# Performance work log

Hardware: AMD Instinct MI355X
Metric: run time of the kernel (lower is better)

The kernel has to match this reference:

```python
import jax, jax.numpy as jnp
import numpy as np

EPS = 1e-5  # BatchNorm eps

def _gcn_norm(edge_index, edge_weight, n):
    # PyG gcn_norm with add_self_loops=True, fill_value=1.0
    loop = jnp.arange(n, dtype=edge_index.dtype)
    row = jnp.concatenate([edge_index[0], loop])
    col = jnp.concatenate([edge_index[1], loop])
    ew = jnp.concatenate([edge_weight, jnp.ones((n,), edge_weight.dtype)])
    deg = jax.ops.segment_sum(ew, col, num_segments=n)
    dis = jnp.where(deg > 0, jax.lax.rsqrt(jnp.maximum(deg, 1e-30)), 0.0)
    norm = dis[row] * ew * dis[col]
    return row, col, norm

def _gcn_conv(x, W, b, row, col, norm, n):
    h = x @ W                               # [N, out]
    msg = h[row] * norm[:, None]            # gather + edge scale
    out = jax.ops.segment_sum(msg, col, num_segments=n)
    return out + b

def _bn_eval(x, gamma, beta, mean, var):
    return (x - mean) * jax.lax.rsqrt(var + EPS) * gamma + beta

def setup_inputs() -> dict:
    key = jax.random.key(0)
    ks = jax.random.split(key, 12)
    N, E, V, H = 100000, 1600000, 256, 128
    x = jax.random.normal(ks[0], (N, V), jnp.float32)
    edge_index = jax.random.randint(ks[1], (2, E), 0, N, jnp.int64)
    edge_weight = jax.random.uniform(ks[2], (E,), jnp.float32)
    s = lambda fan: 1.0 / np.sqrt(fan)
    return {
        "x": x, "edge_index": edge_index, "edge_weight": edge_weight,
        "W1": jax.random.normal(ks[3], (V, H), jnp.float32) * s(V),
        "b1": jnp.zeros((H,), jnp.float32),
        "W2": jax.random.normal(ks[4], (H, H), jnp.float32) * s(H),
        "b2": jnp.zeros((H,), jnp.float32),
        "W3": jax.random.normal(ks[5], (H, 1), jnp.float32) * s(H),
        "b3": jnp.zeros((1,), jnp.float32),
        "Wres": jax.random.normal(ks[6], (V, H), jnp.float32) * s(V),
        "g1": jnp.ones((H,), jnp.float32), "be1": jnp.zeros((H,), jnp.float32),
        "m1": jax.random.normal(ks[7], (H,), jnp.float32) * 0.01,
        "v1": jnp.ones((H,), jnp.float32),
        "g2": jnp.ones((H,), jnp.float32), "be2": jnp.zeros((H,), jnp.float32),
        "m2": jax.random.normal(ks[8], (H,), jnp.float32) * 0.01,
        "v2": jnp.ones((H,), jnp.float32),
    }

def reference(x, edge_index, edge_weight, W1, b1, W2, b2, W3, b3, Wres,
              g1, be1, m1, v1, g2, be2, m2, v2):
    n = x.shape[0]
    row, col, norm = _gcn_norm(edge_index, edge_weight, n)
    res = x @ Wres                                   # residual branch
    h = _gcn_conv(x, W1, b1, row, col, norm, n)
    h = jax.nn.relu(_bn_eval(h, g1, be1, m1, v1))    # dropout off (eval)
    h = _gcn_conv(h, W2, b2, row, col, norm, n) + res
    h = jax.nn.relu(_bn_eval(h, g2, be2, m2, v2))
    h = _gcn_conv(h, W3, b3, row, col, norm, n)      # [N, 1]
    return jnp.squeeze(h, axis=1)
```

## Files before the change

### kernel.cpp

```cpp
#include <hip/hip_runtime.h>
#include <hip/hip_bf16.h>

#define BN_EPS 1e-5f

using short8 = __attribute__((ext_vector_type(8))) short;
using f32x4  = __attribute__((ext_vector_type(4))) float;

#define FIX_SCALE 1048576.0f
#define FIX_MASK  ((1ULL << 42) - 1)
#define CNT_ONE   (1ULL << 42)

static __device__ __forceinline__ unsigned short f2bf(float f) {
  unsigned int u = __float_as_uint(f);
  unsigned int r = (u + 0x7fffu + ((u >> 16) & 1u)) >> 16;
  return (unsigned short)r;
}


static __global__ void hist_kernel(const int* __restrict__ col,
                                   const float* __restrict__ ew,
                                   unsigned long long* __restrict__ packed, int E) {
  int e = blockIdx.x * blockDim.x + threadIdx.x;
  if (e < E) {
    int c = col[e];
    unsigned long long fx = (unsigned long long)(unsigned int)(ew[e] * FIX_SCALE + 0.5f);
    atomicAdd(&packed[c], CNT_ONE | fx);
  }
}

static __global__ void unpack_kernel(const unsigned long long* __restrict__ packed,
                                     float* __restrict__ dis, int* __restrict__ cnt, int N) {
  int i = blockIdx.x * blockDim.x + threadIdx.x;
  if (i < N) {
    unsigned long long v = packed[i];
    cnt[i] = (int)(v >> 42);
    float deg = 1.0f + (float)(v & FIX_MASK) * (1.0f / FIX_SCALE);
    dis[i] = rsqrtf(deg);
  }
}

#define SCAN_B 256
#define SCAN_I 4
static __global__ void scanA(const int* __restrict__ cnt, int* __restrict__ start,
                             int* __restrict__ blkSum, int N) {
  __shared__ int sh[SCAN_B];
  int t = threadIdx.x;
  int base = blockIdx.x * SCAN_B * SCAN_I + t * SCAN_I;
  int v[SCAN_I];
  int tot = 0;
#pragma unroll
  for (int j = 0; j < SCAN_I; ++j) {
    v[j] = (base + j < N) ? cnt[base + j] : 0;
    tot += v[j];
  }
  sh[t] = tot;
  __syncthreads();
  int self = tot;
  for (int off = 1; off < SCAN_B; off <<= 1) {
    int add = (t >= off) ? sh[t - off] : 0;
    __syncthreads();
    sh[t] += add;
    __syncthreads();
  }
  int excl = sh[t] - self;
  if (t == SCAN_B - 1) blkSum[blockIdx.x] = sh[t];
  int run = excl;
#pragma unroll
  for (int j = 0; j < SCAN_I; ++j) {
    if (base + j < N) start[base + j] = run;
    run += v[j];
  }
}

static __global__ void scanB(const int* __restrict__ blkSum, int* __restrict__ blkOff, int nb) {
  __shared__ int sh[256];
  int t = threadIdx.x;
  int v = (t < nb) ? blkSum[t] : 0;
  sh[t] = v;
  __syncthreads();
  for (int off = 1; off < 256; off <<= 1) {
    int add = (t >= off) ? sh[t - off] : 0;
    __syncthreads();
    sh[t] += add;
    __syncthreads();
  }
  if (t < nb) blkOff[t] = sh[t] - v;
}

static __global__ void scanC(int* start, int* cursor, const int* __restrict__ blkOff, int N) {
  int i = blockIdx.x * blockDim.x + threadIdx.x;
  if (i < N) {
    int s = start[i] + blkOff[i / (SCAN_B * SCAN_I)];
    start[i] = s;
    cursor[i] = s;
  }
}

static __global__ void scatter_kernel(const int* __restrict__ row, const int* __restrict__ col,
                                      const float* __restrict__ ew, const float* __restrict__ dis,
                                      int* cursor, int2* __restrict__ edges, int E) {
  int e = blockIdx.x * blockDim.x + threadIdx.x;
  if (e < E) {
    int r = row[e], c = col[e];
    int pos = atomicAdd(&cursor[c], 1);
    float nrm = dis[r] * ew[e] * dis[c];
    edges[pos] = make_int2(r, __float_as_int(nrm));
  }
}


static __global__ void cast_weights(const float* __restrict__ W1, const float* __restrict__ Wres,
                                    const float* __restrict__ W2,
                                    unsigned short* __restrict__ BT1,
                                    unsigned short* __restrict__ BT2) {
  int i = blockIdx.x * blockDim.x + threadIdx.x;
  if (i < 256 * 256) {
    int n = i >> 8, k = i & 255;
    float v = (n < 128) ? W1[k * 128 + n] : Wres[k * 128 + (n - 128)];
    BT1[i] = f2bf(v);
  } else if (i < 256 * 256 + 128 * 128) {
    int j = i - 256 * 256;
    int n = j >> 7, k = j & 127;
    BT2[j] = f2bf(W2[k * 128 + n]);
  }
}


static __global__ __launch_bounds__(256)
void gemm1_mfma(const float* __restrict__ A, const unsigned short* __restrict__ BT,
                unsigned short* __restrict__ C0, float* __restrict__ C1, int M) {
  __shared__ unsigned short As[64 * 40];
  __shared__ unsigned short Bs[256 * 40];
  int t = threadIdx.x;
  int wv = t >> 6, lane = t & 63;
  int quad = lane >> 4, l15 = lane & 15;
  int m0 = blockIdx.x * 64;

  f32x4 acc[4][4];
#pragma unroll
  for (int i = 0; i < 4; ++i)
#pragma unroll
    for (int j = 0; j < 4; ++j) acc[i][j] = (f32x4){0.f, 0.f, 0.f, 0.f};

  int ar = t >> 2;
  int ac = (t & 3) * 8;
  bool avalid = (m0 + ar) < M;
  const float* Arow = A + (size_t)(m0 + ar) * 256 + ac;
  const unsigned short* Brow = BT + (size_t)t * 256;

  for (int k0 = 0; k0 < 256; k0 += 32) {
    float4 a0 = make_float4(0.f, 0.f, 0.f, 0.f), a1 = a0;
    if (avalid) {
      a0 = *(const float4*)(Arow + k0);
      a1 = *(const float4*)(Arow + k0 + 4);
    }
    short8 av;
    av[0] = (short)f2bf(a0.x); av[1] = (short)f2bf(a0.y);
    av[2] = (short)f2bf(a0.z); av[3] = (short)f2bf(a0.w);
    av[4] = (short)f2bf(a1.x); av[5] = (short)f2bf(a1.y);
    av[6] = (short)f2bf(a1.z); av[7] = (short)f2bf(a1.w);
    *(short8*)&As[ar * 40 + ac] = av;

    short8 b0 = *(const short8*)(Brow + k0);
    short8 b1 = *(const short8*)(Brow + k0 + 8);
    short8 b2 = *(const short8*)(Brow + k0 + 16);
    short8 b3 = *(const short8*)(Brow + k0 + 24);
    *(short8*)&Bs[t * 40 + 0]  = b0;
    *(short8*)&Bs[t * 40 + 8]  = b1;
    *(short8*)&Bs[t * 40 + 16] = b2;
    *(short8*)&Bs[t * 40 + 24] = b3;
    __syncthreads();

    short8 af[4], bf[4];
#pragma unroll
    for (int mt = 0; mt < 4; ++mt)
      af[mt] = *(const short8*)&As[(mt * 16 + l15) * 40 + quad * 8];
#pragma unroll
    for (int nt = 0; nt < 4; ++nt)
      bf[nt] = *(const short8*)&Bs[(wv * 64 + nt * 16 + l15) * 40 + quad * 8];
#pragma unroll
    for (int mt = 0; mt < 4; ++mt)
#pragma unroll
      for (int nt = 0; nt < 4; ++nt)
        acc[mt][nt] = __builtin_amdgcn_mfma_f32_16x16x32_bf16(af[mt], bf[nt], acc[mt][nt], 0, 0, 0);
    __syncthreads();
  }

  int nbase = wv * 64;
#pragma unroll
  for (int mt = 0; mt < 4; ++mt) {
#pragma unroll
    for (int nt = 0; nt < 4; ++nt) {
      int n = nbase + nt * 16 + l15;
#pragma unroll
      for (int reg = 0; reg < 4; ++reg) {
        size_t m = (size_t)(m0 + mt * 16 + quad * 4 + reg);
        if (nbase < 128) C0[m * 128 + n] = f2bf(acc[mt][nt][reg]);
        else             C1[m * 128 + (n - 128)] = acc[mt][nt][reg];
      }
    }
  }
}


static __global__ __launch_bounds__(256)
void gemm2_mfma(const unsigned short* __restrict__ A, const unsigned short* __restrict__ BT,
                unsigned short* __restrict__ C, int Mp) {
  __shared__ unsigned short As[128 * 40];
  __shared__ unsigned short Bs[128 * 40];
  int t = threadIdx.x;
  int wv = t >> 6, lane = t & 63;
  int quad = lane >> 4, l15 = lane & 15;
  int m0 = blockIdx.x * 128;

  f32x4 acc[4][4];
#pragma unroll
  for (int i = 0; i < 4; ++i)
#pragma unroll
    for (int j = 0; j < 4; ++j) acc[i][j] = (f32x4){0.f, 0.f, 0.f, 0.f};

  int sr = t >> 1, sc = (t & 1) * 16;

  for (int k0 = 0; k0 < 128; k0 += 32) {
    short8 a0 = *(const short8*)(A + (size_t)(m0 + sr) * 128 + k0 + sc);
    short8 a1 = *(const short8*)(A + (size_t)(m0 + sr) * 128 + k0 + sc + 8);
    *(short8*)&As[sr * 40 + sc]     = a0;
    *(short8*)&As[sr * 40 + sc + 8] = a1;
    short8 b0 = *(const short8*)(BT + (size_t)sr * 128 + k0 + sc);
    short8 b1 = *(const short8*)(BT + (size_t)sr * 128 + k0 + sc + 8);
    *(short8*)&Bs[sr * 40 + sc]     = b0;
    *(short8*)&Bs[sr * 40 + sc + 8] = b1;
    __syncthreads();

    int mb = (wv >> 1) * 64, nb = (wv & 1) * 64;
    short8 af[4], bf[4];
#pragma unroll
    for (int mt = 0; mt < 4; ++mt)
      af[mt] = *(const short8*)&As[(mb + mt * 16 + l15) * 40 + quad * 8];
#pragma unroll
    for (int nt = 0; nt < 4; ++nt)
      bf[nt] = *(const short8*)&Bs[(nb + nt * 16 + l15) * 40 + quad * 8];
#pragma unroll
    for (int mt = 0; mt < 4; ++mt)
#pragma unroll
      for (int nt = 0; nt < 4; ++nt)
        acc[mt][nt] = __builtin_amdgcn_mfma_f32_16x16x32_bf16(af[mt], bf[nt], acc[mt][nt], 0, 0, 0);
    __syncthreads();
  }

  int mb = (wv >> 1) * 64, nb = (wv & 1) * 64;
#pragma unroll
  for (int mt = 0; mt < 4; ++mt)
#pragma unroll
    for (int nt = 0; nt < 4; ++nt) {
      int n = nb + nt * 16 + l15;
#pragma unroll
      for (int reg = 0; reg < 4; ++reg) {
        size_t m = (size_t)(m0 + mb + mt * 16 + quad * 4 + reg);
        C[m * 128 + n] = f2bf(acc[mt][nt][reg]);
      }
    }
  (void)Mp;
}


#define PROP_GATHER_BODY                                                        \
  int c0 = lane * 2;                                                            \
  float d = dis[w];                                                             \
  float d2 = d * d;                                                             \
  float acc0, acc1;                                                             \
  {                                                                             \
    unsigned int u = Hsrc[(size_t)w * 64 + lane];                               \
    acc0 = d2 * __uint_as_float(u << 16);                                       \
    acc1 = d2 * __uint_as_float(u & 0xffff0000u);                               \
  }                                                                             \
  int s = start[w], n = cnt[w];                                                 \
  int k = 0;                                                                    \
  while (k < n) {                                                               \
    int chunk = min(n - k, 64);                                                 \
    int idx = 0;                                                                \
    float wt = 0.f;                                                             \
    if (lane < chunk) {                                                         \
      int2 ev = edges[s + k + lane];                                            \
      idx = ev.x;                                                               \
      wt  = __int_as_float(ev.y);                                               \
    }                                                                           \
    for (int j = 0; j < chunk; j += 8) {                                        \
      int   i0 = __shfl(idx, j + 0, 64), i1 = __shfl(idx, j + 1, 64);           \
      int   i2 = __shfl(idx, j + 2, 64), i3 = __shfl(idx, j + 3, 64);           \
      int   i4 = __shfl(idx, j + 4, 64), i5 = __shfl(idx, j + 5, 64);           \
      int   i6 = __shfl(idx, j + 6, 64), i7 = __shfl(idx, j + 7, 64);           \
      float w0 = __shfl(wt, j + 0, 64), w1 = __shfl(wt, j + 1, 64);             \
      float w2 = __shfl(wt, j + 2, 64), w3 = __shfl(wt, j + 3, 64);             \
      float w4 = __shfl(wt, j + 4, 64), w5 = __shfl(wt, j + 5, 64);             \
      float w6 = __shfl(wt, j + 6, 64), w7 = __shfl(wt, j + 7, 64);             \
      unsigned int u0 = Hsrc[(size_t)i0 * 64 + lane];                           \
      unsigned int u1 = Hsrc[(size_t)i1 * 64 + lane];                           \
      unsigned int u2 = Hsrc[(size_t)i2 * 64 + lane];                           \
      unsigned int u3 = Hsrc[(size_t)i3 * 64 + lane];                           \
      unsigned int u4 = Hsrc[(size_t)i4 * 64 + lane];                           \
      unsigned int u5 = Hsrc[(size_t)i5 * 64 + lane];                           \
      unsigned int u6 = Hsrc[(size_t)i6 * 64 + lane];                           \
      unsigned int u7 = Hsrc[(size_t)i7 * 64 + lane];                           \
      acc0 = fmaf(w0, __uint_as_float(u0 << 16), acc0);                         \
      acc1 = fmaf(w0, __uint_as_float(u0 & 0xffff0000u), acc1);                 \
      acc0 = fmaf(w1, __uint_as_float(u1 << 16), acc0);                         \
      acc1 = fmaf(w1, __uint_as_float(u1 & 0xffff0000u), acc1);                 \
      acc0 = fmaf(w2, __uint_as_float(u2 << 16), acc0);                         \
      acc1 = fmaf(w2, __uint_as_float(u2 & 0xffff0000u), acc1);                 \
      acc0 = fmaf(w3, __uint_as_float(u3 << 16), acc0);                         \
      acc1 = fmaf(w3, __uint_as_float(u3 & 0xffff0000u), acc1);                 \
      acc0 = fmaf(w4, __uint_as_float(u4 << 16), acc0);                         \
      acc1 = fmaf(w4, __uint_as_float(u4 & 0xffff0000u), acc1);                 \
      acc0 = fmaf(w5, __uint_as_float(u5 << 16), acc0);                         \
      acc1 = fmaf(w5, __uint_as_float(u5 & 0xffff0000u), acc1);                 \
      acc0 = fmaf(w6, __uint_as_float(u6 << 16), acc0);                         \
      acc1 = fmaf(w6, __uint_as_float(u6 & 0xffff0000u), acc1);                 \
      acc0 = fmaf(w7, __uint_as_float(u7 << 16), acc0);                         \
      acc1 = fmaf(w7, __uint_as_float(u7 & 0xffff0000u), acc1);                 \
    }                                                                           \
    k += chunk;                                                                 \
  }

static __global__ __launch_bounds__(256)
void prop128_bf16out(const unsigned int* __restrict__ Hsrc,
                     const int* __restrict__ start, const int* __restrict__ cnt,
                     const int2* __restrict__ edges,
                     const float* __restrict__ dis,
                     const float* __restrict__ bvec,
                     const float* __restrict__ g, const float* __restrict__ be,
                     const float* __restrict__ mean, const float* __restrict__ var,
                     unsigned int* __restrict__ Outb, int N) {
  int w = (int)((blockIdx.x * blockDim.x + threadIdx.x) >> 6);
  int lane = threadIdx.x & 63;
  if (w >= N) return;
  PROP_GATHER_BODY
  float x0 = acc0 + bvec[c0];
  float x1 = acc1 + bvec[c0 + 1];
  float s0 = g[c0] * rsqrtf(var[c0] + BN_EPS);
  float s1 = g[c0 + 1] * rsqrtf(var[c0 + 1] + BN_EPS);
  x0 = fmaxf((x0 - mean[c0]) * s0 + be[c0], 0.f);
  x1 = fmaxf((x1 - mean[c0 + 1]) * s1 + be[c0 + 1], 0.f);
  unsigned int packed = (unsigned int)f2bf(x0) | ((unsigned int)f2bf(x1) << 16);
  Outb[(size_t)w * 64 + lane] = packed;
}

static __global__ __launch_bounds__(256)
void prop128_w3out(const unsigned int* __restrict__ Hsrc,
                   const int* __restrict__ start, const int* __restrict__ cnt,
                   const int2* __restrict__ edges,
                   const float* __restrict__ dis,
                   const float* __restrict__ bvec,
                   const float* __restrict__ g, const float* __restrict__ be,
                   const float* __restrict__ mean, const float* __restrict__ var,
                   const float* __restrict__ res, const float* __restrict__ W3,
                   float* __restrict__ h3, int N) {
  int w = (int)((blockIdx.x * blockDim.x + threadIdx.x) >> 6);
  int lane = threadIdx.x & 63;
  if (w >= N) return;
  PROP_GATHER_BODY
  float x0 = acc0 + bvec[c0] + res[(size_t)w * 128 + c0];
  float x1 = acc1 + bvec[c0 + 1] + res[(size_t)w * 128 + c0 + 1];
  float s0 = g[c0] * rsqrtf(var[c0] + BN_EPS);
  float s1 = g[c0 + 1] * rsqrtf(var[c0 + 1] + BN_EPS);
  x0 = fmaxf((x0 - mean[c0]) * s0 + be[c0], 0.f);
  x1 = fmaxf((x1 - mean[c0 + 1]) * s1 + be[c0 + 1], 0.f);
  float v = x0 * W3[c0] + x1 * W3[c0 + 1];
#pragma unroll
  for (int off = 32; off > 0; off >>= 1) v += __shfl_down(v, off, 64);
  if (lane == 0) h3[w] = v;
}


static __global__ void prop3_kernel(const float* __restrict__ h3,
                                    const int* __restrict__ start, const int* __restrict__ cnt,
                                    const int2* __restrict__ edges,
                                    const float* __restrict__ dis, const float* __restrict__ b3,
                                    float* __restrict__ out, int N) {
  int i = blockIdx.x * blockDim.x + threadIdx.x;
  if (i >= N) return;
  float d = dis[i];
  float acc = d * d * h3[i];
  int s = start[i], n = cnt[i];
  for (int k = 0; k < n; ++k) {
    int2 ev = edges[s + k];
    acc = fmaf(__int_as_float(ev.y), h3[ev.x], acc);
  }
  out[i] = acc + b3[0];
}


extern "C" void kernel_launch(void* const* d_in, const int* in_sizes, int n_in,
                              void* d_out, int out_size, void* d_ws, size_t ws_size,
                              hipStream_t stream) {
  const float* x    = (const float*)d_in[0];
  const int*   ei   = (const int*)d_in[1];
  const float* ew   = (const float*)d_in[2];
  const float* W1   = (const float*)d_in[3];
  const float* b1   = (const float*)d_in[4];
  const float* W2   = (const float*)d_in[5];
  const float* b2   = (const float*)d_in[6];
  const float* W3   = (const float*)d_in[7];
  const float* b3   = (const float*)d_in[8];
  const float* Wres = (const float*)d_in[9];
  const float* g1   = (const float*)d_in[10];
  const float* be1  = (const float*)d_in[11];
  const float* m1   = (const float*)d_in[12];
  const float* v1   = (const float*)d_in[13];
  const float* g2   = (const float*)d_in[14];
  const float* be2  = (const float*)d_in[15];
  const float* m2   = (const float*)d_in[16];
  const float* v2   = (const float*)d_in[17];

  int Hh = in_sizes[4];
  int V  = in_sizes[3] / Hh;
  int N  = in_sizes[0] / V;
  int E  = in_sizes[2];
  const int* row = ei;
  const int* col = ei + E;

  int Mp = ((N + 127) / 128) * 128;

  char* p = (char*)d_ws;
  auto alloc = [&](size_t bytes) -> char* {
    char* r = p;
    p += (bytes + 255) & ~(size_t)255;
    return r;
  };
  unsigned long long* packed = (unsigned long long*)alloc((size_t)N * 8);
  float* dis    = (float*)alloc((size_t)N * 4);
  int*   cnt    = (int*)  alloc((size_t)N * 4);
  int*   startA = (int*)  alloc((size_t)N * 4);
  int*   cursor = (int*)  alloc((size_t)N * 4);
  int*   blkSum = (int*)  alloc(256 * 4);
  int*   blkOff = (int*)  alloc(256 * 4);
  int2*  edges  = (int2*) alloc((size_t)E * 8);
  float* h3     = (float*)alloc((size_t)N * 4);
  unsigned short* BT1 = (unsigned short*)alloc((size_t)256 * 256 * 2);
  unsigned short* BT2 = (unsigned short*)alloc((size_t)128 * 128 * 2);
  unsigned short* bufG  = (unsigned short*)alloc((size_t)Mp * 128 * 2);
  unsigned short* bufH1 = (unsigned short*)alloc((size_t)Mp * 128 * 2);
  float* bufRes = (float*)alloc((size_t)Mp * 128 * 4);
  (void)ws_size; (void)n_in; (void)out_size;

  int TB = 256;
  hipMemsetAsync(packed, 0, (size_t)N * 8, stream);
  hist_kernel<<<(E + TB - 1) / TB, TB, 0, stream>>>(col, ew, packed, E);
  unpack_kernel<<<(N + TB - 1) / TB, TB, 0, stream>>>(packed, dis, cnt, N);

  int nb = (N + SCAN_B * SCAN_I - 1) / (SCAN_B * SCAN_I);
  scanA<<<nb, SCAN_B, 0, stream>>>(cnt, startA, blkSum, N);
  scanB<<<1, 256, 0, stream>>>(blkSum, blkOff, nb);
  scanC<<<(N + TB - 1) / TB, TB, 0, stream>>>(startA, cursor, blkOff, N);
  scatter_kernel<<<(E + TB - 1) / TB, TB, 0, stream>>>(row, col, ew, dis, cursor, edges, E);

  cast_weights<<<(256 * 256 + 128 * 128 + TB - 1) / TB, TB, 0, stream>>>(W1, Wres, W2, BT1, BT2);

  gemm1_mfma<<<Mp / 64, 256, 0, stream>>>(x, BT1, bufG, bufRes, N);

  int propBlocks = (int)(((size_t)N * 64 + TB - 1) / TB);
  prop128_bf16out<<<propBlocks, TB, 0, stream>>>((const unsigned int*)bufG, startA, cnt,
                                                 edges, dis, b1, g1, be1, m1, v1,
                                                 (unsigned int*)bufH1, N);

  gemm2_mfma<<<Mp / 128, 256, 0, stream>>>(bufH1, BT2, bufG, Mp);

  prop128_w3out<<<propBlocks, TB, 0, stream>>>((const unsigned int*)bufG, startA, cnt,
                                               edges, dis, b2, g2, be2, m2, v2,
                                               bufRes, W3, h3, N);

  prop3_kernel<<<(N + TB - 1) / TB, TB, 0, stream>>>(h3, startA, cnt, edges,
                                                     dis, b3, (float*)d_out, N);
}
```

Measured before the change: 553.4 us.

## Capture per-edge rank in histogram atomics and drop scatter atomics in CSR build

The histogram atomic now returns the previous count, and that value is stored as a 16-bit rank for each edge. The placement kernel then computes each edge's slot as start plus rank instead of doing a second atomicAdd on a cursor array, and writes it with a nontemporal store. The destination-side dis factor is moved out of the per-edge weight and applied once per node after aggregation. Together these remove E contended atomics and a cursor array, at the cost of an extra E*2-byte rank buffer; rank is truncated to 16 bits, which is only safe for in-degrees below 65536.

```diff
diff --git a/kernel.cpp b/kernel.cpp
--- a/kernel.cpp
+++ b/kernel.cpp
@@ -19,12 +19,14 @@
 
 static __global__ void hist_kernel(const int* __restrict__ col,
                                    const float* __restrict__ ew,
-                                   unsigned long long* __restrict__ packed, int E) {
+                                   unsigned long long* __restrict__ packed,
+                                   unsigned short* __restrict__ rank, int E) {
   int e = blockIdx.x * blockDim.x + threadIdx.x;
   if (e < E) {
     int c = col[e];
     unsigned long long fx = (unsigned long long)(unsigned int)(ew[e] * FIX_SCALE + 0.5f);
-    atomicAdd(&packed[c], CNT_ONE | fx);
+    unsigned long long old = atomicAdd(&packed[c], CNT_ONE | fx);
+    rank[e] = (unsigned short)(old >> 42);
   }
 }
 
@@ -87,24 +89,23 @@
   if (t < nb) blkOff[t] = sh[t] - v;
 }
 
-static __global__ void scanC(int* start, int* cursor, const int* __restrict__ blkOff, int N) {
+static __global__ void scanC(int* start, const int* __restrict__ blkOff, int N) {
   int i = blockIdx.x * blockDim.x + threadIdx.x;
-  if (i < N) {
-    int s = start[i] + blkOff[i / (SCAN_B * SCAN_I)];
-    start[i] = s;
-    cursor[i] = s;
-  }
-}
-
-static __global__ void scatter_kernel(const int* __restrict__ row, const int* __restrict__ col,
-                                      const float* __restrict__ ew, const float* __restrict__ dis,
-                                      int* cursor, int2* __restrict__ edges, int E) {
+  if (i < N) start[i] += blkOff[i / (SCAN_B * SCAN_I)];
+}
+
+static __global__ void place_kernel(const int* __restrict__ row, const int* __restrict__ col,
+                                    const float* __restrict__ ew, const float* __restrict__ dis,
+                                    const int* __restrict__ start,
+                                    const unsigned short* __restrict__ rank,
+                                    long long* __restrict__ edges, int E) {
   int e = blockIdx.x * blockDim.x + threadIdx.x;
   if (e < E) {
     int r = row[e], c = col[e];
-    int pos = atomicAdd(&cursor[c], 1);
-    float nrm = dis[r] * ew[e] * dis[c];
-    edges[pos] = make_int2(r, __float_as_int(nrm));
+    int pos = start[c] + (int)rank[e];
+    float nrm = dis[r] * ew[e];
+    long long v = ((long long)__float_as_int(nrm) << 32) | (unsigned int)r;
+    __builtin_nontemporal_store(v, &edges[pos]);
   }
 }
 
@@ -267,12 +268,11 @@
 #define PROP_GATHER_BODY                                                        \
   int c0 = lane * 2;                                                            \
   float d = dis[w];                                                             \
-  float d2 = d * d;                                                             \
   float acc0, acc1;                                                             \
   {                                                                             \
     unsigned int u = Hsrc[(size_t)w * 64 + lane];                               \
-    acc0 = d2 * __uint_as_float(u << 16);                                       \
-    acc1 = d2 * __uint_as_float(u & 0xffff0000u);                               \
+    acc0 = d * __uint_as_float(u << 16);                                        \
+    acc1 = d * __uint_as_float(u & 0xffff0000u);                                \
   }                                                                             \
   int s = start[w], n = cnt[w];                                                 \
   int k = 0;                                                                    \
@@ -281,9 +281,9 @@
     int idx = 0;                                                                \
     float wt = 0.f;                                                             \
     if (lane < chunk) {                                                         \
-      int2 ev = edges[s + k + lane];                                            \
-      idx = ev.x;                                                               \
-      wt  = __int_as_float(ev.y);                                               \
+      long long ev = edges[s + k + lane];                                       \
+      idx = (int)(unsigned int)(ev & 0xffffffffLL);                             \
+      wt  = __int_as_float((int)(ev >> 32));                                    \
     }                                                                           \
     for (int j = 0; j < chunk; j += 8) {                                        \
       int   i0 = __shfl(idx, j + 0, 64), i1 = __shfl(idx, j + 1, 64);           \
@@ -320,12 +320,14 @@
       acc1 = fmaf(w7, __uint_as_float(u7 & 0xffff0000u), acc1);                 \
     }                                                                           \
     k += chunk;                                                                 \
-  }
+  }                                                                             \
+  acc0 *= d;                                                                    \
+  acc1 *= d;
 
 static __global__ __launch_bounds__(256)
 void prop128_bf16out(const unsigned int* __restrict__ Hsrc,
                      const int* __restrict__ start, const int* __restrict__ cnt,
-                     const int2* __restrict__ edges,
+                     const long long* __restrict__ edges,
                      const float* __restrict__ dis,
                      const float* __restrict__ bvec,
                      const float* __restrict__ g, const float* __restrict__ be,
@@ -348,7 +350,7 @@
 static __global__ __launch_bounds__(256)
 void prop128_w3out(const unsigned int* __restrict__ Hsrc,
                    const int* __restrict__ start, const int* __restrict__ cnt,
-                   const int2* __restrict__ edges,
+                   const long long* __restrict__ edges,
                    const float* __restrict__ dis,
                    const float* __restrict__ bvec,
                    const float* __restrict__ g, const float* __restrict__ be,
@@ -374,19 +376,21 @@
 
 static __global__ void prop3_kernel(const float* __restrict__ h3,
                                     const int* __restrict__ start, const int* __restrict__ cnt,
-                                    const int2* __restrict__ edges,
+                                    const long long* __restrict__ edges,
                                     const float* __restrict__ dis, const float* __restrict__ b3,
                                     float* __restrict__ out, int N) {
   int i = blockIdx.x * blockDim.x + threadIdx.x;
   if (i >= N) return;
   float d = dis[i];
-  float acc = d * d * h3[i];
+  float acc = d * h3[i];
   int s = start[i], n = cnt[i];
   for (int k = 0; k < n; ++k) {
-    int2 ev = edges[s + k];
-    acc = fmaf(__int_as_float(ev.y), h3[ev.x], acc);
-  }
-  out[i] = acc + b3[0];
+    long long ev = edges[s + k];
+    int src = (int)(unsigned int)(ev & 0xffffffffLL);
+    float wt = __int_as_float((int)(ev >> 32));
+    acc = fmaf(wt, h3[src], acc);
+  }
+  out[i] = acc * d + b3[0];
 }
 
 
@@ -431,10 +435,10 @@
   float* dis    = (float*)alloc((size_t)N * 4);
   int*   cnt    = (int*)  alloc((size_t)N * 4);
   int*   startA = (int*)  alloc((size_t)N * 4);
-  int*   cursor = (int*)  alloc((size_t)N * 4);
   int*   blkSum = (int*)  alloc(256 * 4);
   int*   blkOff = (int*)  alloc(256 * 4);
-  int2*  edges  = (int2*) alloc((size_t)E * 8);
+  unsigned short* rank = (unsigned short*)alloc((size_t)E * 2);
+  long long* edges = (long long*)alloc((size_t)E * 8);
   float* h3     = (float*)alloc((size_t)N * 4);
   unsigned short* BT1 = (unsigned short*)alloc((size_t)256 * 256 * 2);
   unsigned short* BT2 = (unsigned short*)alloc((size_t)128 * 128 * 2);
@@ -445,14 +449,14 @@
 
   int TB = 256;
   hipMemsetAsync(packed, 0, (size_t)N * 8, stream);
-  hist_kernel<<<(E + TB - 1) / TB, TB, 0, stream>>>(col, ew, packed, E);
+  hist_kernel<<<(E + TB - 1) / TB, TB, 0, stream>>>(col, ew, packed, rank, E);
   unpack_kernel<<<(N + TB - 1) / TB, TB, 0, stream>>>(packed, dis, cnt, N);
 
   int nb = (N + SCAN_B * SCAN_I - 1) / (SCAN_B * SCAN_I);
   scanA<<<nb, SCAN_B, 0, stream>>>(cnt, startA, blkSum, N);
   scanB<<<1, 256, 0, stream>>>(blkSum, blkOff, nb);
-  scanC<<<(N + TB - 1) / TB, TB, 0, stream>>>(startA, cursor, blkOff, N);
-  scatter_kernel<<<(E + TB - 1) / TB, TB, 0, stream>>>(row, col, ew, dis, cursor, edges, E);
+  scanC<<<(N + TB - 1) / TB, TB, 0, stream>>>(startA, blkOff, N);
+  place_kernel<<<(E + TB - 1) / TB, TB, 0, stream>>>(row, col, ew, dis, startA, rank, edges, E);
 
   cast_weights<<<(256 * 256 + 128 * 128 + TB - 1) / TB, TB, 0, stream>>>(W1, Wres, W2, BT1, BT2);
 
```

New measurement: 527.1 us. 1.05x faster.
